# Optimization experiments

Hardware: AMD Instinct MI355X
Metric: run time of the kernel (lower is better)

Reference implementation:

```python
import jax, jax.numpy as jnp
import numpy as np

B, H, S, D = 2, 16, 2048, 128
TEMPERATURE = 11.313708498984761  # sqrt(128)


def setup_inputs() -> dict:
    key = jax.random.key(0)
    kq, kk, kv = jax.random.split(key, 3)
    q = jax.random.normal(kq, (B, H, S, D), dtype=jnp.float32)
    k = jax.random.normal(kk, (B, H, S, D), dtype=jnp.float32)
    v = jax.random.normal(kv, (B, H, S, D), dtype=jnp.float32)
    # causal (lower-triangular) mask; 0 == masked, matching mask.eq(0) semantics
    mask = jnp.broadcast_to(
        jnp.tril(jnp.ones((S, S), dtype=jnp.int32))[None, None], (B, 1, S, S)
    )
    return {"q": q, "k": k, "v": v, "mask": mask}


def reference(q, k, v, mask):
    # attn = q @ k^T / temperature   -> [B,H,S,S]
    attn = jnp.einsum("bhqd,bhkd->bhqk", q, k) / TEMPERATURE
    masked = mask == 0  # True where masked out
    attn = jnp.where(masked, -jnp.inf, attn)
    attn = jax.nn.softmax(attn, axis=-1)
    attn = jnp.where(masked, 0.0, attn)
    # output = attn @ v -> [B,H,S,D]
    return jnp.einsum("bhqk,bhkd->bhqd", attn, v)
```

## Files before the change

### kernel.cpp

```cpp
#include <hip/hip_runtime.h>
#include <hip/hip_bf16.h>

#define NB   2
#define NH   16
#define NBH  (NB*NH)
#define SEQ  2048
#define DH   128

#define KBLK 64
#define QB   64
#define QW   16
#define KS   136
#define VS   72
#define PS   72

typedef short  short8    __attribute__((ext_vector_type(8)));
typedef unsigned short ushort8_t __attribute__((ext_vector_type(8)));
typedef float  f32x4     __attribute__((ext_vector_type(4)));

constexpr float INV_T = 0.08838834764831845f;
constexpr float LOG2E = 1.4426950408889634f;
constexpr float QSCL  = INV_T * LOG2E;
constexpr float NEG   = -1e30f;

__device__ __forceinline__ unsigned short f2b(float x) {
    union { float f; unsigned u; } c; c.f = x;
    unsigned r = c.u + 0x7FFFu + ((c.u >> 16) & 1u);
    return (unsigned short)(r >> 16);
}

__device__ __forceinline__ void gload_lds16(const void* g, void* l) {
    __builtin_amdgcn_global_load_lds(
        (const __attribute__((address_space(1))) unsigned int*)g,
        (__attribute__((address_space(3))) unsigned int*)l, 16, 0, 0);
}

__global__ __launch_bounds__(256)
void prep_k(const float* __restrict__ K, unsigned short* __restrict__ Kb) {
    size_t i = ((size_t)blockIdx.x * 256 + threadIdx.x) * 8;
    float4 a = *(const float4*)(K + i);
    float4 b = *(const float4*)(K + i + 4);
    ushort8_t o;
    o[0]=f2b(a.x); o[1]=f2b(a.y); o[2]=f2b(a.z); o[3]=f2b(a.w);
    o[4]=f2b(b.x); o[5]=f2b(b.y); o[6]=f2b(b.z); o[7]=f2b(b.w);
    *(ushort8_t*)(Kb + i) = o;
}

__global__ __launch_bounds__(256)
void prep_v(const float* __restrict__ V, unsigned short* __restrict__ Vt) {
    __shared__ unsigned short T[64][72];
    const int bid = blockIdx.x;
    const int dt = bid & 1, st = (bid >> 1) & 31, bh = bid >> 6;
    const int s0 = st * 64, d0 = dt * 64;
    const float* vb = V + (size_t)bh * SEQ * DH;
    const int tid = threadIdx.x;
    #pragma unroll
    for (int u = 0; u < 4; ++u) {
        int f = tid + 256 * u;
        int sl = f >> 4, c4 = f & 15;
        float4 x = *(const float4*)(vb + (size_t)(s0 + sl) * DH + d0 + c4 * 4);
        T[c4*4+0][sl] = f2b(x.x); T[c4*4+1][sl] = f2b(x.y);
        T[c4*4+2][sl] = f2b(x.z); T[c4*4+3][sl] = f2b(x.w);
    }
    __syncthreads();
    unsigned short* vo = Vt + (size_t)bh * DH * SEQ;
    const int dr = tid >> 2, ch = tid & 3;
    ushort8_t w0 = *(const ushort8_t*)&T[dr][ch*16];
    ushort8_t w1 = *(const ushort8_t*)&T[dr][ch*16 + 8];
    *(ushort8_t*)(vo + (size_t)(d0+dr)*SEQ + s0 + ch*16)     = w0;
    *(ushort8_t*)(vo + (size_t)(d0+dr)*SEQ + s0 + ch*16 + 8) = w1;
}

__global__ __launch_bounds__(256, 2)
void attn_fwd2(const float* __restrict__ Q,
               const unsigned short* __restrict__ Kb,
               const unsigned short* __restrict__ Vt,
               float* __restrict__ O)
{
    __shared__ __align__(16) unsigned short Ksh[2][64 * 128];
    __shared__ __align__(16) unsigned short Vsh[2][128 * 64];
    __shared__ __align__(16) unsigned short Psh[4][QW * PS];

    const int bid  = blockIdx.x;
    const int pair = bid & 15;
    const int bh   = bid >> 4;
    const int tid  = threadIdx.x;
    const int wid  = tid >> 6;
    const int lane = tid & 63;
    const int l15  = lane & 15;
    const int l4   = lane >> 4;
    const int rx   = l15 & 7;

    const size_t base = (size_t)bh * SEQ * DH;
    const unsigned short* Kbh = Kb + base;
    const unsigned short* Vth = Vt + base;

    auto stage = [&](int bufi, int tt) {
        const int kv0 = tt * KBLK;
        {
            const int sl = lane & 15, rr = lane >> 4;
            #pragma unroll
            for (int i = 0; i < 4; ++i) {
                int row = wid * 16 + i * 4 + rr;
                int ss  = sl ^ (row & 7);
                gload_lds16(Kbh + (size_t)(kv0 + row) * DH + ss * 8,
                            &Ksh[bufi][(wid * 16 + i * 4) * 128]);
            }
        }
        {
            const int sl = lane & 7, rr = lane >> 3;
            #pragma unroll
            for (int i = 0; i < 4; ++i) {
                int row = wid * 32 + i * 8 + rr;
                int ss  = sl ^ (row & 7);
                gload_lds16(Vth + (size_t)row * SEQ + kv0 + ss * 8,
                            &Vsh[bufi][(wid * 32 + i * 8) * 64]);
            }
        }
    };

    for (int ph = 0; ph < 2; ++ph) {
        const int qblk  = ph ? (31 - pair) : pair;
        const int qbase = qblk * 64 + wid * QW;
        const int nt    = qblk + 1;

        short8 aq[4];
        {
            const float* qp = Q + base + (size_t)(qbase + l15) * DH + 8 * l4;
            #pragma unroll
            for (int kb = 0; kb < 4; ++kb) {
                float4 x0 = *(const float4*)(qp + 32 * kb);
                float4 x1 = *(const float4*)(qp + 32 * kb + 4);
                short8 a;
                a[0] = (short)f2b(x0.x * QSCL); a[1] = (short)f2b(x0.y * QSCL);
                a[2] = (short)f2b(x0.z * QSCL); a[3] = (short)f2b(x0.w * QSCL);
                a[4] = (short)f2b(x1.x * QSCL); a[5] = (short)f2b(x1.y * QSCL);
                a[6] = (short)f2b(x1.z * QSCL); a[7] = (short)f2b(x1.w * QSCL);
                aq[kb] = a;
            }
        }

        f32x4 acc[8];
        #pragma unroll
        for (int i = 0; i < 8; ++i) acc[i] = (f32x4){0.f, 0.f, 0.f, 0.f};
        float mrun[4], lrun[4];
        #pragma unroll
        for (int j = 0; j < 4; ++j) { mrun[j] = NEG; lrun[j] = 0.f; }

        __syncthreads();
        stage(0, 0);

        for (int t = 0; t < nt; ++t) {
            const int cur = t & 1;
            const int kvb = t * KBLK;
            asm volatile("s_waitcnt vmcnt(0)" ::: "memory");
            __syncthreads();
            if (t + 1 < nt) stage(cur ^ 1, t + 1);

            if (kvb <= qbase + QW - 1) {
                const unsigned short* Kc = Ksh[cur];
                const unsigned short* Vc = Vsh[cur];

                f32x4 sf[4];
                #pragma unroll
                for (int f = 0; f < 4; ++f) {
                    f32x4 c = (f32x4){0.f, 0.f, 0.f, 0.f};
                    const int row = 16 * f + l15;
                    #pragma unroll
                    for (int kb = 0; kb < 4; ++kb) {
                        short8 bk = *(const short8*)&Kc[row * 128 + ((4 * kb + l4) ^ rx) * 8];
                        c = __builtin_amdgcn_mfma_f32_16x16x32_bf16(aq[kb], bk, c, 0, 0, 0);
                    }
                    sf[f] = c;
                }

                float pmax[4] = {NEG, NEG, NEG, NEG};
                if (kvb + KBLK - 1 > qbase) {
                    #pragma unroll
                    for (int f = 0; f < 4; ++f) {
                        const int col = kvb + 16 * f + l15;
                        #pragma unroll
                        for (int j = 0; j < 4; ++j) {
                            const int row = qbase + 4 * l4 + j;
                            float val = (col <= row) ? sf[f][j] : NEG;
                            sf[f][j] = val;
                            pmax[j] = fmaxf(pmax[j], val);
                        }
                    }
                } else {
                    #pragma unroll
                    for (int f = 0; f < 4; ++f)
                        #pragma unroll
                        for (int j = 0; j < 4; ++j)
                            pmax[j] = fmaxf(pmax[j], sf[f][j]);
                }
                #pragma unroll
                for (int j = 0; j < 4; ++j) {
                    #pragma unroll
                    for (int off = 8; off > 0; off >>= 1)
                        pmax[j] = fmaxf(pmax[j], __shfl_xor(pmax[j], off));
                }
                float scl[4], rsum[4];
                #pragma unroll
                for (int j = 0; j < 4; ++j) {
                    float mn = fmaxf(mrun[j], pmax[j]);
                    scl[j]  = exp2f(mrun[j] - mn);
                    mrun[j] = mn;
                    rsum[j] = 0.f;
                }
                #pragma unroll
                for (int f = 0; f < 4; ++f) {
                    #pragma unroll
                    for (int j = 0; j < 4; ++j) {
                        float pv = exp2f(sf[f][j] - mrun[j]);
                        sf[f][j] = pv;
                        rsum[j] += pv;
                    }
                }
                #pragma unroll
                for (int j = 0; j < 4; ++j) {
                    #pragma unroll
                    for (int off = 8; off > 0; off >>= 1)
                        rsum[j] += __shfl_xor(rsum[j], off);
                    lrun[j] = lrun[j] * scl[j] + rsum[j];
                }
                #pragma unroll
                for (int i = 0; i < 8; ++i)
                    #pragma unroll
                    for (int j = 0; j < 4; ++j)
                        acc[i][j] *= scl[j];

                #pragma unroll
                for (int f = 0; f < 4; ++f)
                    #pragma unroll
                    for (int j = 0; j < 4; ++j)
                        Psh[wid][(4 * l4 + j) * PS + 16 * f + l15] = f2b(sf[f][j]);

                #pragma unroll
                for (int kb = 0; kb < 2; ++kb) {
                    short8 pa = *(const short8*)&Psh[wid][l15 * PS + 32 * kb + 8 * l4];
                    #pragma unroll
                    for (int db = 0; db < 8; ++db) {
                        const int row = 16 * db + l15;
                        short8 bv = *(const short8*)&Vc[row * 64 + ((4 * kb + l4) ^ rx) * 8];
                        acc[db] = __builtin_amdgcn_mfma_f32_16x16x32_bf16(pa, bv, acc[db], 0, 0, 0);
                    }
                }
            }
        }

        float inv[4];
        #pragma unroll
        for (int j = 0; j < 4; ++j) inv[j] = 1.f / lrun[j];
        float* op = O + base + (size_t)qbase * DH;
        #pragma unroll
        for (int db = 0; db < 8; ++db)
            #pragma unroll
            for (int j = 0; j < 4; ++j)
                op[(size_t)(4 * l4 + j) * DH + 16 * db + l15] = acc[db][j] * inv[j];
    }
}

__global__ __launch_bounds__(256)
void attn_fwd(const float* __restrict__ Q, const float* __restrict__ K,
              const float* __restrict__ V, float* __restrict__ O)
{
    __shared__ __align__(16) unsigned short KshL[KBLK * KS];
    __shared__ __align__(16) unsigned short VshL[DH * VS];
    __shared__ __align__(16) unsigned short PshL[4][QW * PS];

    const int bid  = blockIdx.x;
    const int qblk = bid & 31;
    const int bh   = bid >> 5;
    const int tid  = threadIdx.x;
    const int wid  = tid >> 6;
    const int lane = tid & 63;
    const int l15  = lane & 15;
    const int l4   = lane >> 4;

    const size_t base  = (size_t)bh * SEQ * DH;
    const int    qbase = qblk * QB + wid * QW;

    short8 aq[4];
    {
        const float* qp = Q + base + (size_t)(qbase + l15) * DH + 8 * l4;
        #pragma unroll
        for (int kb = 0; kb < 4; ++kb) {
            float4 x0 = *(const float4*)(qp + 32 * kb);
            float4 x1 = *(const float4*)(qp + 32 * kb + 4);
            short8 a;
            a[0] = (short)f2b(x0.x * INV_T); a[1] = (short)f2b(x0.y * INV_T);
            a[2] = (short)f2b(x0.z * INV_T); a[3] = (short)f2b(x0.w * INV_T);
            a[4] = (short)f2b(x1.x * INV_T); a[5] = (short)f2b(x1.y * INV_T);
            a[6] = (short)f2b(x1.z * INV_T); a[7] = (short)f2b(x1.w * INV_T);
            aq[kb] = a;
        }
    }
    f32x4 acc[8];
    #pragma unroll
    for (int i = 0; i < 8; ++i) acc[i] = (f32x4){0.f, 0.f, 0.f, 0.f};
    float mrun[4], lrun[4];
    #pragma unroll
    for (int j = 0; j < 4; ++j) { mrun[j] = NEG; lrun[j] = 0.f; }

    const int ntiles = qblk + 1;
    for (int t = 0; t < ntiles; ++t) {
        const int kvb = t * KBLK;
        #pragma unroll
        for (int i = 0; i < 8; ++i) {
            int f  = tid + 256 * i;
            int kv = f >> 5, c4 = f & 31;
            float4 x = *(const float4*)(K + base + (size_t)(kvb + kv) * DH + 4 * c4);
            ushort4 b4;
            b4.x = f2b(x.x); b4.y = f2b(x.y); b4.z = f2b(x.z); b4.w = f2b(x.w);
            *(ushort4*)&KshL[kv * KS + 4 * c4] = b4;
        }
        {
            const int dd  = tid & 127;
            const int kvg = (tid >> 7) * 8;
            #pragma unroll
            for (int p = 0; p < 4; ++p) {
                const int kvL = p * 16 + kvg;
                const float* vp = V + base + (size_t)(kvb + kvL) * DH + dd;
                float x[8];
                #pragma unroll
                for (int j = 0; j < 8; ++j) x[j] = vp[(size_t)j * DH];
                ushort4 lo, hi;
                lo.x = f2b(x[0]); lo.y = f2b(x[1]); lo.z = f2b(x[2]); lo.w = f2b(x[3]);
                hi.x = f2b(x[4]); hi.y = f2b(x[5]); hi.z = f2b(x[6]); hi.w = f2b(x[7]);
                *(ushort4*)&VshL[dd * VS + kvL]     = lo;
                *(ushort4*)&VshL[dd * VS + kvL + 4] = hi;
            }
        }
        __syncthreads();
        if (kvb <= qbase + QW - 1) {
            f32x4 sf[4];
            #pragma unroll
            for (int f = 0; f < 4; ++f) {
                f32x4 c = (f32x4){0.f, 0.f, 0.f, 0.f};
                #pragma unroll
                for (int kb = 0; kb < 4; ++kb) {
                    short8 bk = *(const short8*)&KshL[(16 * f + l15) * KS + 32 * kb + 8 * l4];
                    c = __builtin_amdgcn_mfma_f32_16x16x32_bf16(aq[kb], bk, c, 0, 0, 0);
                }
                sf[f] = c;
            }
            float pmax[4] = {NEG, NEG, NEG, NEG};
            #pragma unroll
            for (int f = 0; f < 4; ++f) {
                const int col = kvb + 16 * f + l15;
                #pragma unroll
                for (int j = 0; j < 4; ++j) {
                    const int row = qbase + 4 * l4 + j;
                    float val = (col <= row) ? sf[f][j] : NEG;
                    sf[f][j] = val;
                    pmax[j] = fmaxf(pmax[j], val);
                }
            }
            #pragma unroll
            for (int j = 0; j < 4; ++j) {
                #pragma unroll
                for (int off = 8; off > 0; off >>= 1)
                    pmax[j] = fmaxf(pmax[j], __shfl_xor(pmax[j], off));
            }
            float scl[4], rsum[4];
            #pragma unroll
            for (int j = 0; j < 4; ++j) {
                float mn = fmaxf(mrun[j], pmax[j]);
                scl[j]  = exp2f((mrun[j] - mn) * LOG2E);
                mrun[j] = mn;
                rsum[j] = 0.f;
            }
            #pragma unroll
            for (int f = 0; f < 4; ++f) {
                #pragma unroll
                for (int j = 0; j < 4; ++j) {
                    float pv = exp2f((sf[f][j] - mrun[j]) * LOG2E);
                    sf[f][j] = pv;
                    rsum[j] += pv;
                }
            }
            #pragma unroll
            for (int j = 0; j < 4; ++j) {
                #pragma unroll
                for (int off = 8; off > 0; off >>= 1)
                    rsum[j] += __shfl_xor(rsum[j], off);
                lrun[j] = lrun[j] * scl[j] + rsum[j];
            }
            #pragma unroll
            for (int i = 0; i < 8; ++i)
                #pragma unroll
                for (int j = 0; j < 4; ++j)
                    acc[i][j] *= scl[j];
            #pragma unroll
            for (int f = 0; f < 4; ++f)
                #pragma unroll
                for (int j = 0; j < 4; ++j)
                    PshL[wid][(4 * l4 + j) * PS + 16 * f + l15] = f2b(sf[f][j]);
            #pragma unroll
            for (int kb = 0; kb < 2; ++kb) {
                short8 pa = *(const short8*)&PshL[wid][l15 * PS + 32 * kb + 8 * l4];
                #pragma unroll
                for (int db = 0; db < 8; ++db) {
                    short8 bv = *(const short8*)&VshL[(16 * db + l15) * VS + 32 * kb + 8 * l4];
                    acc[db] = __builtin_amdgcn_mfma_f32_16x16x32_bf16(pa, bv, acc[db], 0, 0, 0);
                }
            }
        }
        __syncthreads();
    }
    float inv[4];
    #pragma unroll
    for (int j = 0; j < 4; ++j) inv[j] = 1.f / lrun[j];
    float* op = O + base + (size_t)qbase * DH;
    #pragma unroll
    for (int db = 0; db < 8; ++db)
        #pragma unroll
        for (int j = 0; j < 4; ++j)
            op[(size_t)(4 * l4 + j) * DH + 16 * db + l15] = acc[db][j] * inv[j];
}

extern "C" void kernel_launch(void* const* d_in, const int* in_sizes, int n_in,
                              void* d_out, int out_size, void* d_ws, size_t ws_size,
                              hipStream_t stream) {
    const float* q = (const float*)d_in[0];
    const float* k = (const float*)d_in[1];
    const float* v = (const float*)d_in[2];
    float* o = (float*)d_out;

    const size_t elems = (size_t)NBH * SEQ * DH;
    const size_t need  = elems * 2 * sizeof(unsigned short);
    if (ws_size >= need) {
        unsigned short* Kb = (unsigned short*)d_ws;
        unsigned short* Vt = Kb + elems;
        prep_k<<<dim3((unsigned)(elems / (256 * 8))), dim3(256), 0, stream>>>(k, Kb);
        prep_v<<<dim3(NBH * (SEQ / 64) * (DH / 64)), dim3(256), 0, stream>>>(v, Vt);
        attn_fwd2<<<dim3(NBH * 16), dim3(256), 0, stream>>>(q, Kb, Vt, o);
    } else {
        attn_fwd<<<dim3(NBH * 32), dim3(256), 0, stream>>>(q, k, v, o);
    }
}
```

Measured before the change: 248.5 us.

## Transpose MFMA operands so each lane owns one query row, drop P LDS round-trip

Swaps the MFMA A/B operands so the score tile is transposed and each lane holds one query row. Row max and sum then need only two cross-lane shuffles, and running max/sum become scalars per lane. P is repacked to bf16 through register shuffles instead of a shared-memory write and read, and the output is written with float4 stores. It also adds a lazy rescale that updates the max only when it grows by more than 8 in log2 units, plus setprio around the MFMA sections; the removed guard skipping fully masked tiles may add a little work.

```diff
diff --git a/kernel.cpp b/kernel.cpp
--- a/kernel.cpp
+++ b/kernel.cpp
@@ -17,16 +17,22 @@
 typedef short  short8    __attribute__((ext_vector_type(8)));
 typedef unsigned short ushort8_t __attribute__((ext_vector_type(8)));
 typedef float  f32x4     __attribute__((ext_vector_type(4)));
+typedef int    int4v     __attribute__((ext_vector_type(4)));
 
 constexpr float INV_T = 0.08838834764831845f;
 constexpr float LOG2E = 1.4426950408889634f;
 constexpr float QSCL  = INV_T * LOG2E;
 constexpr float NEG   = -1e30f;
+constexpr float DEFER = 8.0f;
 
 __device__ __forceinline__ unsigned short f2b(float x) {
     union { float f; unsigned u; } c; c.f = x;
     unsigned r = c.u + 0x7FFFu + ((c.u >> 16) & 1u);
     return (unsigned short)(r >> 16);
+}
+
+__device__ __forceinline__ unsigned pack2(float lo, float hi) {
+    return (unsigned)f2b(lo) | ((unsigned)f2b(hi) << 16);
 }
 
 __device__ __forceinline__ void gload_lds16(const void* g, void* l) {
@@ -79,7 +85,6 @@
 {
     __shared__ __align__(16) unsigned short Ksh[2][64 * 128];
     __shared__ __align__(16) unsigned short Vsh[2][128 * 64];
-    __shared__ __align__(16) unsigned short Psh[4][QW * PS];
 
     const int bid  = blockIdx.x;
     const int pair = bid & 15;
@@ -90,6 +95,9 @@
     const int l15  = lane & 15;
     const int l4   = lane >> 4;
     const int rx   = l15 & 7;
+    const int hi   = l4 >> 1;
+    const int srcA = l15 + 16 * ((2 * l4) & 3);
+    const int srcB = l15 + 16 * ((2 * l4 + 1) & 3);
 
     const size_t base = (size_t)bh * SEQ * DH;
     const unsigned short* Kbh = Kb + base;
@@ -123,10 +131,11 @@
         const int qblk  = ph ? (31 - pair) : pair;
         const int qbase = qblk * 64 + wid * QW;
         const int nt    = qblk + 1;
+        const int qrow  = qbase + l15;
 
         short8 aq[4];
         {
-            const float* qp = Q + base + (size_t)(qbase + l15) * DH + 8 * l4;
+            const float* qp = Q + base + (size_t)qrow * DH + 8 * l4;
             #pragma unroll
             for (int kb = 0; kb < 4; ++kb) {
                 float4 x0 = *(const float4*)(qp + 32 * kb);
@@ -143,9 +152,7 @@
         f32x4 acc[8];
         #pragma unroll
         for (int i = 0; i < 8; ++i) acc[i] = (f32x4){0.f, 0.f, 0.f, 0.f};
-        float mrun[4], lrun[4];
-        #pragma unroll
-        for (int j = 0; j < 4; ++j) { mrun[j] = NEG; lrun[j] = 0.f; }
+        float mrun = NEG, lrun = 0.f;
 
         __syncthreads();
         stage(0, 0);
@@ -157,107 +164,116 @@
             __syncthreads();
             if (t + 1 < nt) stage(cur ^ 1, t + 1);
 
-            if (kvb <= qbase + QW - 1) {
-                const unsigned short* Kc = Ksh[cur];
-                const unsigned short* Vc = Vsh[cur];
-
-                f32x4 sf[4];
-                #pragma unroll
-                for (int f = 0; f < 4; ++f) {
-                    f32x4 c = (f32x4){0.f, 0.f, 0.f, 0.f};
-                    const int row = 16 * f + l15;
-                    #pragma unroll
-                    for (int kb = 0; kb < 4; ++kb) {
-                        short8 bk = *(const short8*)&Kc[row * 128 + ((4 * kb + l4) ^ rx) * 8];
-                        c = __builtin_amdgcn_mfma_f32_16x16x32_bf16(aq[kb], bk, c, 0, 0, 0);
-                    }
-                    sf[f] = c;
-                }
-
-                float pmax[4] = {NEG, NEG, NEG, NEG};
-                if (kvb + KBLK - 1 > qbase) {
-                    #pragma unroll
-                    for (int f = 0; f < 4; ++f) {
-                        const int col = kvb + 16 * f + l15;
-                        #pragma unroll
-                        for (int j = 0; j < 4; ++j) {
-                            const int row = qbase + 4 * l4 + j;
-                            float val = (col <= row) ? sf[f][j] : NEG;
-                            sf[f][j] = val;
-                            pmax[j] = fmaxf(pmax[j], val);
-                        }
-                    }
-                } else {
-                    #pragma unroll
-                    for (int f = 0; f < 4; ++f)
-                        #pragma unroll
-                        for (int j = 0; j < 4; ++j)
-                            pmax[j] = fmaxf(pmax[j], sf[f][j]);
-                }
-                #pragma unroll
-                for (int j = 0; j < 4; ++j) {
-                    #pragma unroll
-                    for (int off = 8; off > 0; off >>= 1)
-                        pmax[j] = fmaxf(pmax[j], __shfl_xor(pmax[j], off));
-                }
-                float scl[4], rsum[4];
-                #pragma unroll
-                for (int j = 0; j < 4; ++j) {
-                    float mn = fmaxf(mrun[j], pmax[j]);
-                    scl[j]  = exp2f(mrun[j] - mn);
-                    mrun[j] = mn;
-                    rsum[j] = 0.f;
-                }
+            const unsigned short* Kc = Ksh[cur];
+            const unsigned short* Vc = Vsh[cur];
+
+            f32x4 sf[4];
+            __builtin_amdgcn_s_setprio(1);
+            #pragma unroll
+            for (int f = 0; f < 4; ++f) {
+                f32x4 c = (f32x4){0.f, 0.f, 0.f, 0.f};
+                const int row = 16 * f + l15;
+                #pragma unroll
+                for (int kb = 0; kb < 4; ++kb) {
+                    short8 bk = *(const short8*)&Kc[row * 128 + ((4 * kb + l4) ^ rx) * 8];
+                    c = __builtin_amdgcn_mfma_f32_16x16x32_bf16(bk, aq[kb], c, 0, 0, 0);
+                }
+                sf[f] = c;
+            }
+            __builtin_amdgcn_s_setprio(0);
+
+            if (kvb + KBLK - 1 > qbase) {
                 #pragma unroll
                 for (int f = 0; f < 4; ++f) {
                     #pragma unroll
                     for (int j = 0; j < 4; ++j) {
-                        float pv = exp2f(sf[f][j] - mrun[j]);
-                        sf[f][j] = pv;
-                        rsum[j] += pv;
+                        const int kv = kvb + 16 * f + 4 * l4 + j;
+                        if (kv > qrow) sf[f][j] = NEG;
                     }
                 }
-                #pragma unroll
-                for (int j = 0; j < 4; ++j) {
-                    #pragma unroll
-                    for (int off = 8; off > 0; off >>= 1)
-                        rsum[j] += __shfl_xor(rsum[j], off);
-                    lrun[j] = lrun[j] * scl[j] + rsum[j];
-                }
+            }
+
+            float pmax;
+            {
+                float m0 = fmaxf(fmaxf(sf[0][0], sf[0][1]), fmaxf(sf[0][2], sf[0][3]));
+                float m1 = fmaxf(fmaxf(sf[1][0], sf[1][1]), fmaxf(sf[1][2], sf[1][3]));
+                float m2 = fmaxf(fmaxf(sf[2][0], sf[2][1]), fmaxf(sf[2][2], sf[2][3]));
+                float m3 = fmaxf(fmaxf(sf[3][0], sf[3][1]), fmaxf(sf[3][2], sf[3][3]));
+                pmax = fmaxf(fmaxf(m0, m1), fmaxf(m2, m3));
+            }
+            pmax = fmaxf(pmax, __shfl_xor(pmax, 16));
+            pmax = fmaxf(pmax, __shfl_xor(pmax, 32));
+
+            if (__any(pmax > mrun + DEFER)) {
+                float mn  = fmaxf(mrun, pmax);
+                float scl = exp2f(mrun - mn);
+                mrun = mn;
+                lrun *= scl;
                 #pragma unroll
                 for (int i = 0; i < 8; ++i)
                     #pragma unroll
                     for (int j = 0; j < 4; ++j)
-                        acc[i][j] *= scl[j];
-
-                #pragma unroll
-                for (int f = 0; f < 4; ++f)
-                    #pragma unroll
-                    for (int j = 0; j < 4; ++j)
-                        Psh[wid][(4 * l4 + j) * PS + 16 * f + l15] = f2b(sf[f][j]);
-
-                #pragma unroll
-                for (int kb = 0; kb < 2; ++kb) {
-                    short8 pa = *(const short8*)&Psh[wid][l15 * PS + 32 * kb + 8 * l4];
-                    #pragma unroll
-                    for (int db = 0; db < 8; ++db) {
-                        const int row = 16 * db + l15;
-                        short8 bv = *(const short8*)&Vc[row * 64 + ((4 * kb + l4) ^ rx) * 8];
-                        acc[db] = __builtin_amdgcn_mfma_f32_16x16x32_bf16(pa, bv, acc[db], 0, 0, 0);
-                    }
-                }
-            }
-        }
-
-        float inv[4];
+                        acc[i][j] *= scl;
+            }
+
+            float rs = 0.f;
+            #pragma unroll
+            for (int f = 0; f < 4; ++f)
+                #pragma unroll
+                for (int j = 0; j < 4; ++j) {
+                    float p = exp2f(sf[f][j] - mrun);
+                    sf[f][j] = p;
+                    rs += p;
+                }
+            rs += __shfl_xor(rs, 16);
+            rs += __shfl_xor(rs, 32);
+            lrun += rs;
+
+            unsigned pd0[4], pd1[4];
+            #pragma unroll
+            for (int f = 0; f < 4; ++f) {
+                pd0[f] = pack2(sf[f][0], sf[f][1]);
+                pd1[f] = pack2(sf[f][2], sf[f][3]);
+            }
+
+            #pragma unroll
+            for (int kb = 0; kb < 2; ++kb) {
+                unsigned sA0 = __shfl(pd0[2*kb],     srcA);
+                unsigned sA1 = __shfl(pd1[2*kb],     srcA);
+                unsigned tA0 = __shfl(pd0[2*kb + 1], srcA);
+                unsigned tA1 = __shfl(pd1[2*kb + 1], srcA);
+                unsigned sB0 = __shfl(pd0[2*kb],     srcB);
+                unsigned sB1 = __shfl(pd1[2*kb],     srcB);
+                unsigned tB0 = __shfl(pd0[2*kb + 1], srcB);
+                unsigned tB1 = __shfl(pd1[2*kb + 1], srcB);
+                int4v w;
+                w[0] = (int)(hi ? tA0 : sA0);
+                w[1] = (int)(hi ? tA1 : sA1);
+                w[2] = (int)(hi ? tB0 : sB0);
+                w[3] = (int)(hi ? tB1 : sB1);
+                short8 pb;
+                __builtin_memcpy(&pb, &w, 16);
+
+                __builtin_amdgcn_s_setprio(1);
+                #pragma unroll
+                for (int db = 0; db < 8; ++db) {
+                    const int row = 16 * db + l15;
+                    short8 bv = *(const short8*)&Vc[row * 64 + ((4 * kb + l4) ^ rx) * 8];
+                    acc[db] = __builtin_amdgcn_mfma_f32_16x16x32_bf16(bv, pb, acc[db], 0, 0, 0);
+                }
+                __builtin_amdgcn_s_setprio(0);
+            }
+        }
+
+        const float inv = 1.f / lrun;
+        float* op = O + base + (size_t)qrow * DH + 4 * l4;
         #pragma unroll
-        for (int j = 0; j < 4; ++j) inv[j] = 1.f / lrun[j];
-        float* op = O + base + (size_t)qbase * DH;
-        #pragma unroll
-        for (int db = 0; db < 8; ++db)
-            #pragma unroll
-            for (int j = 0; j < 4; ++j)
-                op[(size_t)(4 * l4 + j) * DH + 16 * db + l15] = acc[db][j] * inv[j];
+        for (int db = 0; db < 8; ++db) {
+            float4 v;
+            v.x = acc[db][0] * inv; v.y = acc[db][1] * inv;
+            v.z = acc[db][2] * inv; v.w = acc[db][3] * inv;
+            *(float4*)(op + 16 * db) = v;
+        }
     }
 }
 
```

Result: faster. 240.2 us (-3.4%).
